# Kernel tuning notes

Hardware: AMD Instinct MI355X
Metric: run time of the kernel (lower is better)

The kernel has to match this reference:

```python
import jax, jax.numpy as jnp
import numpy as np

ARAP_WEIGHT = 1.0


def _decoder(code, W1, b1, W2, b2, W3, b3):
    # code: [D] -> vertices [N, 3]
    h = jax.nn.relu(code @ W1 + b1)
    h = jax.nn.relu(h @ W2 + b2)
    v = h @ W3 + b3
    return v.reshape(-1, 3)


def _arap_per_vertex(xyz1, recon, nbr, num_nbr, wmat):
    # xyz1, recon: [N,3]; nbr: [N,K] int; num_nbr: [N]; wmat: [N,K]
    N, K = nbr.shape
    mask = (jnp.arange(K)[None, :] < num_nbr[:, None]).astype(wmat.dtype)
    w = wmat * mask                              # zero out padded neighbors
    e_rest = xyz1[nbr] - xyz1[:, None, :]        # [N,K,3] rest-pose edges (gather)
    e_def = recon[nbr] - recon[:, None, :]       # [N,K,3] deformed edges (gather)
    # weighted covariance per vertex: S_i = sum_k w_ik e_ik e'_ik^T  -> [N,3,3]
    S = jnp.einsum('nk,nka,nkb->nab', w, e_rest, e_def)
    U, _, Vt = jnp.linalg.svd(S)
    V = jnp.swapaxes(Vt, -1, -2)
    R0 = jnp.einsum('nab,ncb->nac', V, U)        # V U^T
    d = jnp.linalg.det(R0)                       # reflection fix
    diag = jnp.stack([jnp.ones_like(d), jnp.ones_like(d), d], axis=-1)  # [N,3]
    R = jnp.einsum('nab,nb,ncb->nac', V, diag, U)
    R = jax.lax.stop_gradient(R)                 # local-global: rotations fixed in bwd
    e_rot = jnp.einsum('nab,nkb->nka', R, e_rest)
    resid = e_def - e_rot
    return jnp.sum(w * jnp.sum(resid * resid, axis=-1), axis=-1)  # [N]


def setup_inputs() -> dict:
    key = jax.random.key(0)
    ks = jax.random.split(key, 12)
    N, K, D = 20000, 16, 256
    H1, H2 = 512, 1024
    inp = {
        'code': jax.random.normal(ks[0], (D,), jnp.float32),
        'xyz1': jax.random.normal(ks[1], (N, 3), jnp.float32),
        'weightMatrix': jax.random.uniform(ks[2], (N, K), jnp.float32),
        'W1': jax.random.normal(ks[3], (D, H1), jnp.float32) * (1.0 / np.sqrt(D)),
        'b1': jax.random.normal(ks[4], (H1,), jnp.float32) * 0.01,
        'W2': jax.random.normal(ks[5], (H1, H2), jnp.float32) * (1.0 / np.sqrt(H1)),
        'b2': jax.random.normal(ks[6], (H2,), jnp.float32) * 0.01,
        'W3': jax.random.normal(ks[7], (H2, N * 3), jnp.float32) * (1.0 / np.sqrt(H2)),
        'b3': jax.random.normal(ks[8], (N * 3,), jnp.float32) * 0.01,
        'neighborsMatrix': jax.random.randint(ks[9], (N, K), 0, N, jnp.int64),
        'numNeighbors': jax.random.randint(ks[10], (N,), 0, 17, jnp.int64),
    }
    return inp


def reference(code, xyz1, weightMatrix, W1, b1, W2, b2, W3, b3,
              neighborsMatrix, numNeighbors):
    def energy(c):
        recon = _decoder(c, W1, b1, W2, b2, W3, b3)
        pv = _arap_per_vertex(xyz1, recon, neighborsMatrix, numNeighbors, weightMatrix)
        return ARAP_WEIGHT * jnp.mean(pv)

    E, g = jax.value_and_grad(energy)(code)
    # torch module returns (arapEnergy.item(), -code.grad) with arapEnergy = -E
    return (-E, g)
```

## Files before the change

### kernel.cpp

```cpp
#include <hip/hip_runtime.h>
#include <hip/hip_bf16.h>

#define N_V   20000
#define KNB   16
#define DCODE 256
#define H1    512
#define H2    1024
#define M3    60000

#define OFF_L1P   0
#define OFF_L2P   4096
#define OFF_VPART 12288
#define OFF_V     492288
#define OFF_GV    552288
#define OFF_GZ2   612288
#define OFF_GZ1   613312
#define OFF_H1    613824
#define OFF_H2    614336
#define OFF_HC    615360
#define OFF_LIST  616384
#define OFF_CNT   617408
#define OFF_E     617410
#define OFF_R     617412


__global__ void k_l1p(const float* __restrict__ code, const float* __restrict__ W1,
                      float* __restrict__ ws) {
    int m = blockIdx.x * 256 + threadIdx.x;
    int d0 = blockIdx.y * 32;
    float acc = 0.f;
#pragma unroll
    for (int d = 0; d < 32; ++d)
        acc += code[d0 + d] * W1[(size_t)(d0 + d) * H1 + m];
    ws[OFF_L1P + blockIdx.y * H1 + m] = acc;
    int gid = (blockIdx.y * 2 + blockIdx.x) * 256 + threadIdx.x;
    for (int idx = gid; idx < M3; idx += 4096) ws[OFF_GV + idx] = 0.f;
    if (gid == 0) { ws[OFF_E] = 0.f; ws[OFF_E + 1] = 0.f; }
}

__global__ void k_l2p(const float* __restrict__ b1, const float* __restrict__ W2,
                      float* __restrict__ ws) {
    __shared__ float h1s[64];
    int dz = blockIdx.y, d0 = dz * 64;
    int t = threadIdx.x;
    if (t < 64) {
        float s = b1[d0 + t];
#pragma unroll
        for (int p = 0; p < 8; ++p) s += ws[OFF_L1P + p * H1 + d0 + t];
        float h = fmaxf(s, 0.f);
        h1s[t] = h;
        if (blockIdx.x == 0) ws[OFF_H1 + d0 + t] = h;
    }
    __syncthreads();
    int m = blockIdx.x * 256 + t;
    float acc = 0.f;
#pragma unroll 8
    for (int d = 0; d < 64; ++d)
        acc += h1s[d] * W2[(size_t)(d0 + d) * H2 + m];
    ws[OFF_L2P + dz * H2 + m] = acc;
}

__global__ void k_compact(const float* __restrict__ b2, float* __restrict__ ws) {
    __shared__ int scan[256];
    int t = threadIdx.x;
    float h[4]; int c = 0;
#pragma unroll
    for (int q = 0; q < 4; ++q) {
        int j = t * 4 + q;
        float s = b2[j];
#pragma unroll
        for (int p = 0; p < 8; ++p) s += ws[OFF_L2P + p * H2 + j];
        float hv = fmaxf(s, 0.f);
        ws[OFF_H2 + j] = hv;
        ws[OFF_GZ2 + j] = 0.f;
        h[q] = hv;
        c += (hv > 0.f) ? 1 : 0;
    }
    scan[t] = c;
    __syncthreads();
    for (int off = 1; off < 256; off <<= 1) {
        int x = (t >= off) ? scan[t - off] : 0;
        __syncthreads();
        scan[t] += x;
        __syncthreads();
    }
    int base = scan[t] - c;
    int* list = reinterpret_cast<int*>(&ws[OFF_LIST]);
#pragma unroll
    for (int q = 0; q < 4; ++q) {
        if (h[q] > 0.f) {
            list[base] = t * 4 + q;
            ws[OFF_HC + base] = h[q];
            ++base;
        }
    }
    if (t == 255) *reinterpret_cast<int*>(&ws[OFF_CNT]) = scan[255];
}

__global__ void k_l3p(const float* __restrict__ W3, float* __restrict__ ws) {
    __shared__ int   rlist[128];
    __shared__ float rh[128];
    int jz = blockIdx.y;
    int cnt = *reinterpret_cast<const int*>(&ws[OFF_CNT]);
    int per = (cnt + 7) >> 3;
    int s0 = jz * per;
    int s1 = s0 + per; if (s1 > cnt) s1 = cnt;
    int n = s1 - s0;
    int t = threadIdx.x;
    if (t < 128 && t < n) {
        rlist[t] = reinterpret_cast<const int*>(&ws[OFF_LIST])[s0 + t];
        rh[t]    = ws[OFF_HC + s0 + t];
    }
    __syncthreads();
    int m4 = blockIdx.x * 1024 + t * 4;
    if (m4 >= M3) return;
    float ax = 0.f, ay = 0.f, az = 0.f, aw = 0.f;
    int ii = 0;
    for (; ii + 3 < n; ii += 4) {
        int r0 = rlist[ii], r1 = rlist[ii + 1], r2 = rlist[ii + 2], r3 = rlist[ii + 3];
        float h0 = rh[ii], h1v = rh[ii + 1], h2v = rh[ii + 2], h3 = rh[ii + 3];
        float4 w0 = *reinterpret_cast<const float4*>(&W3[(size_t)r0 * M3 + m4]);
        float4 w1 = *reinterpret_cast<const float4*>(&W3[(size_t)r1 * M3 + m4]);
        float4 w2 = *reinterpret_cast<const float4*>(&W3[(size_t)r2 * M3 + m4]);
        float4 w3 = *reinterpret_cast<const float4*>(&W3[(size_t)r3 * M3 + m4]);
        ax += h0 * w0.x + h1v * w1.x + h2v * w2.x + h3 * w3.x;
        ay += h0 * w0.y + h1v * w1.y + h2v * w2.y + h3 * w3.y;
        az += h0 * w0.z + h1v * w1.z + h2v * w2.z + h3 * w3.z;
        aw += h0 * w0.w + h1v * w1.w + h2v * w2.w + h3 * w3.w;
    }
    for (; ii < n; ++ii) {
        int r0 = rlist[ii]; float h0 = rh[ii];
        float4 w0 = *reinterpret_cast<const float4*>(&W3[(size_t)r0 * M3 + m4]);
        ax += h0 * w0.x; ay += h0 * w0.y; az += h0 * w0.z; aw += h0 * w0.w;
    }
    float4 acc = make_float4(ax, ay, az, aw);
    *reinterpret_cast<float4*>(&ws[OFF_VPART + jz * M3 + m4]) = acc;
}

__global__ void k_vred(const float* __restrict__ b3, float* __restrict__ ws) {
    int i4 = blockIdx.x * 256 + threadIdx.x;
    if (i4 < M3 / 4) {
        int m = i4 * 4;
        float4 a = *reinterpret_cast<const float4*>(&b3[m]);
#pragma unroll
        for (int jz = 0; jz < 8; ++jz) {
            float4 p = *reinterpret_cast<const float4*>(&ws[OFF_VPART + jz * M3 + m]);
            a.x += p.x; a.y += p.y; a.z += p.z; a.w += p.w;
        }
        *reinterpret_cast<float4*>(&ws[OFF_V + m]) = a;
    }
}


__device__ inline void jrotf(float a[3][3], float v[3][3], int p, int q) {
    float apq = a[p][q];
    if (fabsf(apq) < 1e-30f) return;
    float theta = (a[q][q] - a[p][p]) / (2.0f * apq);
    float t;
    if (fabsf(theta) > 1e18f) t = 0.5f / theta;
    else t = copysignf(1.0f, theta) / (fabsf(theta) + sqrtf(theta * theta + 1.0f));
    float c = 1.0f / sqrtf(t * t + 1.0f);
    float s = t * c;
    float app = a[p][p], aqq = a[q][q];
    a[p][p] = app - t * apq;
    a[q][q] = aqq + t * apq;
    a[p][q] = 0.0f; a[q][p] = 0.0f;
    int r = 3 - p - q;
    float arp = a[r][p], arq = a[r][q];
    a[r][p] = c * arp - s * arq; a[p][r] = a[r][p];
    a[r][q] = s * arp + c * arq; a[q][r] = a[r][q];
#pragma unroll
    for (int k2 = 0; k2 < 3; ++k2) {
        float vkp = v[k2][p], vkq = v[k2][q];
        v[k2][p] = c * vkp - s * vkq;
        v[k2][q] = s * vkp + c * vkq;
    }
}

__device__ void compute_Rf(const float S[3][3], float R[3][3]) {
    float A[3][3], V[3][3];
#pragma unroll
    for (int a = 0; a < 3; ++a)
#pragma unroll
        for (int b = 0; b < 3; ++b) {
            float s = 0.0f;
#pragma unroll
            for (int c = 0; c < 3; ++c) s += S[c][a] * S[c][b];
            A[a][b] = s;
            V[a][b] = (a == b) ? 1.0f : 0.0f;
        }
    for (int sweep = 0; sweep < 15; ++sweep) {
        float off = A[0][1]*A[0][1] + A[0][2]*A[0][2] + A[1][2]*A[1][2];
        float dg  = A[0][0]*A[0][0] + A[1][1]*A[1][1] + A[2][2]*A[2][2];
        if (off <= 1e-12f * (dg + 1e-30f)) break;
        jrotf(A, V, 0, 1); jrotf(A, V, 0, 2); jrotf(A, V, 1, 2);
    }
    int id[3] = {0, 1, 2};
    if (A[id[0]][id[0]] < A[id[1]][id[1]]) { int t = id[0]; id[0] = id[1]; id[1] = t; }
    if (A[id[0]][id[0]] < A[id[2]][id[2]]) { int t = id[0]; id[0] = id[2]; id[2] = t; }
    if (A[id[1]][id[1]] < A[id[2]][id[2]]) { int t = id[1]; id[1] = id[2]; id[2] = t; }
    float v0[3], v1[3], v2[3];
#pragma unroll
    for (int r = 0; r < 3; ++r) {
        v0[r] = V[r][id[0]]; v1[r] = V[r][id[1]]; v2[r] = V[r][id[2]];
    }
    float u0[3], u1[3], u2[3];
#pragma unroll
    for (int a = 0; a < 3; ++a)
        u0[a] = S[a][0]*v0[0] + S[a][1]*v0[1] + S[a][2]*v0[2];
    float n0 = sqrtf(u0[0]*u0[0] + u0[1]*u0[1] + u0[2]*u0[2]);
    if (!(n0 > 1e-20f)) {
#pragma unroll
        for (int a = 0; a < 3; ++a)
#pragma unroll
            for (int c = 0; c < 3; ++c) R[a][c] = (a == c) ? 1.0f : 0.0f;
        return;
    }
#pragma unroll
    for (int a = 0; a < 3; ++a) u0[a] /= n0;
    float t1[3];
#pragma unroll
    for (int a = 0; a < 3; ++a)
        t1[a] = S[a][0]*v1[0] + S[a][1]*v1[1] + S[a][2]*v1[2];
    float dp = u0[0]*t1[0] + u0[1]*t1[1] + u0[2]*t1[2];
#pragma unroll
    for (int a = 0; a < 3; ++a) t1[a] -= dp * u0[a];
    float n1 = sqrtf(t1[0]*t1[0] + t1[1]*t1[1] + t1[2]*t1[2]);
    if (n1 > 1e-5f * n0) {
#pragma unroll
        for (int a = 0; a < 3; ++a) u1[a] = t1[a] / n1;
    } else {
        int m = (fabsf(u0[0]) <= fabsf(u0[1]) && fabsf(u0[0]) <= fabsf(u0[2])) ? 0
              : (fabsf(u0[1]) <= fabsf(u0[2]) ? 1 : 2);
        float e[3] = {0.0f, 0.0f, 0.0f}; e[m] = 1.0f;
        float cx[3] = { u0[1]*e[2] - u0[2]*e[1],
                        u0[2]*e[0] - u0[0]*e[2],
                        u0[0]*e[1] - u0[1]*e[0] };
        float nn = sqrtf(cx[0]*cx[0] + cx[1]*cx[1] + cx[2]*cx[2]);
#pragma unroll
        for (int a = 0; a < 3; ++a) u1[a] = cx[a] / nn;
    }
    u2[0] = u0[1]*u1[2] - u0[2]*u1[1];
    u2[1] = u0[2]*u1[0] - u0[0]*u1[2];
    u2[2] = u0[0]*u1[1] - u0[1]*u1[0];
    float d = v0[0]*(v1[1]*v2[2] - v1[2]*v2[1])
            - v0[1]*(v1[0]*v2[2] - v1[2]*v2[0])
            + v0[2]*(v1[0]*v2[1] - v1[1]*v2[0]);
#pragma unroll
    for (int a = 0; a < 3; ++a)
#pragma unroll
        for (int c = 0; c < 3; ++c)
            R[a][c] = v0[a]*u0[c] + v1[a]*u1[c] + d * (v2[a]*u2[c]);
}

__global__ void k_arapR(const float* __restrict__ xyz1, const float* __restrict__ wmat,
                        const int* __restrict__ nbr, const int* __restrict__ nnum,
                        float* __restrict__ ws) {
    int i = blockIdx.x * 64 + threadIdx.x;
    if (i >= N_V) return;
    const float* recon = ws + OFF_V;
    int num = nnum[i]; if (num > KNB) num = KNB;
    float cr0 = xyz1[3*i], cr1 = xyz1[3*i+1], cr2 = xyz1[3*i+2];
    float cd0 = recon[3*i], cd1 = recon[3*i+1], cd2 = recon[3*i+2];
    float S[3][3] = {{0,0,0},{0,0,0},{0,0,0}};
    for (int k = 0; k < num; ++k) {
        int j = nbr[i*KNB + k];
        float w = wmat[i*KNB + k];
        float er0 = xyz1[3*j]   - cr0, er1 = xyz1[3*j+1] - cr1, er2 = xyz1[3*j+2] - cr2;
        float ed0 = recon[3*j]  - cd0, ed1 = recon[3*j+1] - cd1, ed2 = recon[3*j+2] - cd2;
        S[0][0] += w*er0*ed0; S[0][1] += w*er0*ed1; S[0][2] += w*er0*ed2;
        S[1][0] += w*er1*ed0; S[1][1] += w*er1*ed1; S[1][2] += w*er1*ed2;
        S[2][0] += w*er2*ed0; S[2][1] += w*er2*ed1; S[2][2] += w*er2*ed2;
    }
    float R[3][3];
    compute_Rf(S, R);
#pragma unroll
    for (int a = 0; a < 3; ++a)
#pragma unroll
        for (int c = 0; c < 3; ++c)
            ws[OFF_R + (a*3 + c) * N_V + i] = R[a][c];
}

__global__ void k_arapG(const float* __restrict__ xyz1, const float* __restrict__ wmat,
                        const int* __restrict__ nbr, const int* __restrict__ nnum,
                        float* __restrict__ ws) {
    const float* recon = ws + OFF_V;
    float* gv = ws + OFF_GV;
    int i = blockIdx.x * 64 + threadIdx.x;
    double pv = 0.0;
    if (i < N_V) {
        int num = nnum[i]; if (num > KNB) num = KNB;
        float cr0 = xyz1[3*i], cr1 = xyz1[3*i+1], cr2 = xyz1[3*i+2];
        float cd0 = recon[3*i], cd1 = recon[3*i+1], cd2 = recon[3*i+2];
        float R00 = ws[OFF_R + 0*N_V + i], R01 = ws[OFF_R + 1*N_V + i], R02 = ws[OFF_R + 2*N_V + i];
        float R10 = ws[OFF_R + 3*N_V + i], R11 = ws[OFF_R + 4*N_V + i], R12 = ws[OFF_R + 5*N_V + i];
        float R20 = ws[OFF_R + 6*N_V + i], R21 = ws[OFF_R + 7*N_V + i], R22 = ws[OFF_R + 8*N_V + i];
        const float gscale = 2.0f / (float)N_V;
        float own0 = 0.f, own1 = 0.f, own2 = 0.f;
        for (int k = 0; k < num; ++k) {
            int j = nbr[i*KNB + k];
            float w = wmat[i*KNB + k];
            float er0 = xyz1[3*j]   - cr0, er1 = xyz1[3*j+1] - cr1, er2 = xyz1[3*j+2] - cr2;
            float ed0 = recon[3*j]  - cd0, ed1 = recon[3*j+1] - cd1, ed2 = recon[3*j+2] - cd2;
            float r0 = ed0 - (R00*er0 + R01*er1 + R02*er2);
            float r1 = ed1 - (R10*er0 + R11*er1 + R12*er2);
            float r2 = ed2 - (R20*er0 + R21*er1 + R22*er2);
            pv += (double)(w * (r0*r0 + r1*r1 + r2*r2));
            float g0 = gscale * w * r0;
            float g1 = gscale * w * r1;
            float g2 = gscale * w * r2;
            atomicAdd(&gv[3*j+0], g0);
            atomicAdd(&gv[3*j+1], g1);
            atomicAdd(&gv[3*j+2], g2);
            own0 += g0; own1 += g1; own2 += g2;
        }
        if (num > 0) {
            atomicAdd(&gv[3*i+0], -own0);
            atomicAdd(&gv[3*i+1], -own1);
            atomicAdd(&gv[3*i+2], -own2);
        }
    }
#pragma unroll
    for (int m = 32; m; m >>= 1) pv += __shfl_xor(pv, m);
    if (threadIdx.x == 0)
        atomicAdd(reinterpret_cast<double*>(ws + OFF_E), pv);
}


__global__ void k_gh2(const float* __restrict__ W3, float* __restrict__ ws) {
    int b = blockIdx.x;
    int cnt = *reinterpret_cast<const int*>(&ws[OFF_CNT]);
    if (b >= cnt) return;
    int j = reinterpret_cast<const int*>(&ws[OFF_LIST])[b];
    const float4* w3r = reinterpret_cast<const float4*>(W3 + (size_t)j * M3);
    const float4* gv4 = reinterpret_cast<const float4*>(ws + OFF_GV);
    float acc = 0.f;
    for (int it = threadIdx.x; it < M3 / 4; it += 256) {
        float4 a = w3r[it], g = gv4[it];
        acc += a.x*g.x + a.y*g.y + a.z*g.z + a.w*g.w;
    }
    for (int m = 32; m; m >>= 1) acc += __shfl_xor(acc, m);
    __shared__ float wsum[4];
    if ((threadIdx.x & 63) == 0) wsum[threadIdx.x >> 6] = acc;
    __syncthreads();
    if (threadIdx.x == 0) ws[OFF_GZ2 + j] = wsum[0] + wsum[1] + wsum[2] + wsum[3];
}

__global__ void k_gh1(const float* __restrict__ W2, float* __restrict__ ws) {
    int wv = threadIdx.x >> 6, ln = threadIdx.x & 63;
    int i = blockIdx.x * 4 + wv;
    const float* gz2 = ws + OFF_GZ2;
    float acc = 0.f;
#pragma unroll
    for (int it = 0; it < H2 / 64; ++it) {
        int jj = ln + it * 64;
        acc += W2[(size_t)i * H2 + jj] * gz2[jj];
    }
    for (int m = 32; m; m >>= 1) acc += __shfl_xor(acc, m);
    if (ln == 0) ws[OFF_GZ1 + i] = (ws[OFF_H1 + i] > 0.f) ? acc : 0.f;
}

__global__ void k_gcode(const float* __restrict__ W1, float* __restrict__ ws,
                        float* __restrict__ out) {
    int wv = threadIdx.x >> 6, ln = threadIdx.x & 63;
    int d = blockIdx.x * 4 + wv;
    const float* gz1 = ws + OFF_GZ1;
    float acc = 0.f;
#pragma unroll
    for (int it = 0; it < H1 / 64; ++it) {
        int ii = ln + it * 64;
        acc += W1[(size_t)d * H1 + ii] * gz1[ii];
    }
    for (int m = 32; m; m >>= 1) acc += __shfl_xor(acc, m);
    if (ln == 0) out[1 + d] = acc;
    if (blockIdx.x == 0 && threadIdx.x == 0) {
        double E = *reinterpret_cast<const double*>(ws + OFF_E);
        out[0] = (float)(-(E / (double)N_V));
    }
}

extern "C" void kernel_launch(void* const* d_in, const int* in_sizes, int n_in,
                              void* d_out, int out_size, void* d_ws, size_t ws_size,
                              hipStream_t stream) {
    const float* code = (const float*)d_in[0];
    const float* xyz1 = (const float*)d_in[1];
    const float* wmat = (const float*)d_in[2];
    const float* W1   = (const float*)d_in[3];
    const float* b1   = (const float*)d_in[4];
    const float* W2   = (const float*)d_in[5];
    const float* b2   = (const float*)d_in[6];
    const float* W3   = (const float*)d_in[7];
    const float* b3   = (const float*)d_in[8];
    const int*   nbr  = (const int*)d_in[9];
    const int*   nnum = (const int*)d_in[10];
    float* out = (float*)d_out;
    float* ws  = (float*)d_ws;

    k_l1p    <<<dim3(2, 8),  256, 0, stream>>>(code, W1, ws);
    k_l2p    <<<dim3(4, 8),  256, 0, stream>>>(b1, W2, ws);
    k_compact<<<1,           256, 0, stream>>>(b2, ws);
    k_l3p    <<<dim3(59, 8), 256, 0, stream>>>(W3, ws);
    k_vred   <<<59,          256, 0, stream>>>(b3, ws);
    k_arapR  <<<313,          64, 0, stream>>>(xyz1, wmat, nbr, nnum, ws);
    k_arapG  <<<313,          64, 0, stream>>>(xyz1, wmat, nbr, nnum, ws);
    k_gh2    <<<1024,        256, 0, stream>>>(W3, ws);
    k_gh1    <<<128,         256, 0, stream>>>(W2, ws);
    k_gcode  <<<64,          256, 0, stream>>>(W1, ws, out);
}
```

Before: 120.9 us.

## Fuse decoder and ARAP stages to cut kernel launches from ten to six

Result: slower. 143.2 us (+18.4%).

```diff
diff --git a/kernel.cpp b/kernel.cpp
--- a/kernel.cpp
+++ b/kernel.cpp
@@ -8,110 +8,86 @@
 #define H2    1024
 #define M3    60000
 
-#define OFF_L1P   0
-#define OFF_L2P   4096
-#define OFF_VPART 12288
-#define OFF_V     492288
-#define OFF_GV    552288
-#define OFF_GZ2   612288
-#define OFF_GZ1   613312
-#define OFF_H1    613824
-#define OFF_H2    614336
-#define OFF_HC    615360
-#define OFF_LIST  616384
-#define OFF_CNT   617408
-#define OFF_E     617410
-#define OFF_R     617412
-
-
-__global__ void k_l1p(const float* __restrict__ code, const float* __restrict__ W1,
+#define OFF_V     0
+#define OFF_GV    60000
+#define OFF_GZ2   120000
+#define OFF_GZ1   121024
+#define OFF_H1    121536
+#define OFF_H2    122048
+#define OFF_E     123072
+
+__global__ void k_mlp(const float* __restrict__ code, const float* __restrict__ W1,
+                      const float* __restrict__ b1, const float* __restrict__ W2,
+                      const float* __restrict__ b2, const float* __restrict__ b3,
                       float* __restrict__ ws) {
-    int m = blockIdx.x * 256 + threadIdx.x;
-    int d0 = blockIdx.y * 32;
+    __shared__ float h1s[H1];
+    __shared__ float zp[8][32];
+    int t = threadIdx.x;
+
+    for (int mm = t; mm < H1; mm += 256) {
+        float acc = 0.f;
+#pragma unroll 4
+        for (int d = 0; d < DCODE; ++d)
+            acc += code[d] * W1[(size_t)d * H1 + mm];
+        h1s[mm] = fmaxf(acc + b1[mm], 0.f);
+    }
+    __syncthreads();
+    if (blockIdx.x == 0)
+        for (int mm = t; mm < H1; mm += 256) ws[OFF_H1 + mm] = h1s[mm];
+
+    int g = t >> 5, mm = t & 31;
+    int m = blockIdx.x * 32 + mm;
     float acc = 0.f;
-#pragma unroll
-    for (int d = 0; d < 32; ++d)
-        acc += code[d0 + d] * W1[(size_t)(d0 + d) * H1 + m];
-    ws[OFF_L1P + blockIdx.y * H1 + m] = acc;
-    int gid = (blockIdx.y * 2 + blockIdx.x) * 256 + threadIdx.x;
-    for (int idx = gid; idx < M3; idx += 4096) ws[OFF_GV + idx] = 0.f;
+    int d0 = g * 64;
+#pragma unroll 8
+    for (int d = d0; d < d0 + 64; ++d)
+        acc += h1s[d] * W2[(size_t)d * H2 + m];
+    zp[g][mm] = acc;
+    __syncthreads();
+    if (g == 0) {
+        float s = b2[m];
+#pragma unroll
+        for (int p = 0; p < 8; ++p) s += zp[p][mm];
+        ws[OFF_H2 + m] = fmaxf(s, 0.f);
+    }
+
+    int gid = blockIdx.x * 256 + t;
+    for (int idx = gid; idx < M3; idx += 8192) {
+        ws[OFF_V + idx]  = b3[idx];
+        ws[OFF_GV + idx] = 0.f;
+    }
     if (gid == 0) { ws[OFF_E] = 0.f; ws[OFF_E + 1] = 0.f; }
 }
 
-__global__ void k_l2p(const float* __restrict__ b1, const float* __restrict__ W2,
-                      float* __restrict__ ws) {
-    __shared__ float h1s[64];
-    int dz = blockIdx.y, d0 = dz * 64;
+__global__ void k_l3v(const float* __restrict__ W3, float* __restrict__ ws) {
+    __shared__ float rh[128];
+    __shared__ int   rlist[128];
+    __shared__ int   scan[128];
     int t = threadIdx.x;
-    if (t < 64) {
-        float s = b1[d0 + t];
-#pragma unroll
-        for (int p = 0; p < 8; ++p) s += ws[OFF_L1P + p * H1 + d0 + t];
-        float h = fmaxf(s, 0.f);
-        h1s[t] = h;
-        if (blockIdx.x == 0) ws[OFF_H1 + d0 + t] = h;
-    }
-    __syncthreads();
-    int m = blockIdx.x * 256 + t;
-    float acc = 0.f;
-#pragma unroll 8
-    for (int d = 0; d < 64; ++d)
-        acc += h1s[d] * W2[(size_t)(d0 + d) * H2 + m];
-    ws[OFF_L2P + dz * H2 + m] = acc;
-}
-
-__global__ void k_compact(const float* __restrict__ b2, float* __restrict__ ws) {
-    __shared__ int scan[256];
-    int t = threadIdx.x;
-    float h[4]; int c = 0;
-#pragma unroll
-    for (int q = 0; q < 4; ++q) {
-        int j = t * 4 + q;
-        float s = b2[j];
-#pragma unroll
-        for (int p = 0; p < 8; ++p) s += ws[OFF_L2P + p * H2 + j];
-        float hv = fmaxf(s, 0.f);
-        ws[OFF_H2 + j] = hv;
-        ws[OFF_GZ2 + j] = 0.f;
-        h[q] = hv;
-        c += (hv > 0.f) ? 1 : 0;
-    }
-    scan[t] = c;
-    __syncthreads();
-    for (int off = 1; off < 256; off <<= 1) {
-        int x = (t >= off) ? scan[t - off] : 0;
+    int rbase = blockIdx.y * 128;
+
+    float hv = 0.f; int flag = 0;
+    if (t < 128) {
+        hv = ws[OFF_H2 + rbase + t];
+        flag = (hv > 0.f) ? 1 : 0;
+        scan[t] = flag;
+    }
+    __syncthreads();
+    for (int off = 1; off < 128; off <<= 1) {
+        int x = 0;
+        if (t < 128 && t >= off) x = scan[t - off];
         __syncthreads();
-        scan[t] += x;
+        if (t < 128) scan[t] += x;
         __syncthreads();
     }
-    int base = scan[t] - c;
-    int* list = reinterpret_cast<int*>(&ws[OFF_LIST]);
-#pragma unroll
-    for (int q = 0; q < 4; ++q) {
-        if (h[q] > 0.f) {
-            list[base] = t * 4 + q;
-            ws[OFF_HC + base] = h[q];
-            ++base;
-        }
-    }
-    if (t == 255) *reinterpret_cast<int*>(&ws[OFF_CNT]) = scan[255];
-}
-
-__global__ void k_l3p(const float* __restrict__ W3, float* __restrict__ ws) {
-    __shared__ int   rlist[128];
-    __shared__ float rh[128];
-    int jz = blockIdx.y;
-    int cnt = *reinterpret_cast<const int*>(&ws[OFF_CNT]);
-    int per = (cnt + 7) >> 3;
-    int s0 = jz * per;
-    int s1 = s0 + per; if (s1 > cnt) s1 = cnt;
-    int n = s1 - s0;
-    int t = threadIdx.x;
-    if (t < 128 && t < n) {
-        rlist[t] = reinterpret_cast<const int*>(&ws[OFF_LIST])[s0 + t];
-        rh[t]    = ws[OFF_HC + s0 + t];
-    }
-    __syncthreads();
+    if (t < 128 && flag) {
+        int idx = scan[t] - 1;
+        rlist[idx] = rbase + t;
+        rh[idx] = hv;
+    }
+    __syncthreads();
+    int n = scan[127];
+
     int m4 = blockIdx.x * 1024 + t * 4;
     if (m4 >= M3) return;
     float ax = 0.f, ay = 0.f, az = 0.f, aw = 0.f;
@@ -133,22 +109,10 @@
         float4 w0 = *reinterpret_cast<const float4*>(&W3[(size_t)r0 * M3 + m4]);
         ax += h0 * w0.x; ay += h0 * w0.y; az += h0 * w0.z; aw += h0 * w0.w;
     }
-    float4 acc = make_float4(ax, ay, az, aw);
-    *reinterpret_cast<float4*>(&ws[OFF_VPART + jz * M3 + m4]) = acc;
-}
-
-__global__ void k_vred(const float* __restrict__ b3, float* __restrict__ ws) {
-    int i4 = blockIdx.x * 256 + threadIdx.x;
-    if (i4 < M3 / 4) {
-        int m = i4 * 4;
-        float4 a = *reinterpret_cast<const float4*>(&b3[m]);
-#pragma unroll
-        for (int jz = 0; jz < 8; ++jz) {
-            float4 p = *reinterpret_cast<const float4*>(&ws[OFF_VPART + jz * M3 + m]);
-            a.x += p.x; a.y += p.y; a.z += p.z; a.w += p.w;
-        }
-        *reinterpret_cast<float4*>(&ws[OFF_V + m]) = a;
-    }
+    atomicAdd(&ws[OFF_V + m4 + 0], ax);
+    atomicAdd(&ws[OFF_V + m4 + 1], ay);
+    atomicAdd(&ws[OFF_V + m4 + 2], az);
+    atomicAdd(&ws[OFF_V + m4 + 3], aw);
 }
 
 
@@ -253,37 +217,9 @@
             R[a][c] = v0[a]*u0[c] + v1[a]*u1[c] + d * (v2[a]*u2[c]);
 }
 
-__global__ void k_arapR(const float* __restrict__ xyz1, const float* __restrict__ wmat,
-                        const int* __restrict__ nbr, const int* __restrict__ nnum,
-                        float* __restrict__ ws) {
-    int i = blockIdx.x * 64 + threadIdx.x;
-    if (i >= N_V) return;
-    const float* recon = ws + OFF_V;
-    int num = nnum[i]; if (num > KNB) num = KNB;
-    float cr0 = xyz1[3*i], cr1 = xyz1[3*i+1], cr2 = xyz1[3*i+2];
-    float cd0 = recon[3*i], cd1 = recon[3*i+1], cd2 = recon[3*i+2];
-    float S[3][3] = {{0,0,0},{0,0,0},{0,0,0}};
-    for (int k = 0; k < num; ++k) {
-        int j = nbr[i*KNB + k];
-        float w = wmat[i*KNB + k];
-        float er0 = xyz1[3*j]   - cr0, er1 = xyz1[3*j+1] - cr1, er2 = xyz1[3*j+2] - cr2;
-        float ed0 = recon[3*j]  - cd0, ed1 = recon[3*j+1] - cd1, ed2 = recon[3*j+2] - cd2;
-        S[0][0] += w*er0*ed0; S[0][1] += w*er0*ed1; S[0][2] += w*er0*ed2;
-        S[1][0] += w*er1*ed0; S[1][1] += w*er1*ed1; S[1][2] += w*er1*ed2;
-        S[2][0] += w*er2*ed0; S[2][1] += w*er2*ed1; S[2][2] += w*er2*ed2;
-    }
-    float R[3][3];
-    compute_Rf(S, R);
-#pragma unroll
-    for (int a = 0; a < 3; ++a)
-#pragma unroll
-        for (int c = 0; c < 3; ++c)
-            ws[OFF_R + (a*3 + c) * N_V + i] = R[a][c];
-}
-
-__global__ void k_arapG(const float* __restrict__ xyz1, const float* __restrict__ wmat,
-                        const int* __restrict__ nbr, const int* __restrict__ nnum,
-                        float* __restrict__ ws) {
+__global__ void k_arap(const float* __restrict__ xyz1, const float* __restrict__ wmat,
+                       const int* __restrict__ nbr, const int* __restrict__ nnum,
+                       float* __restrict__ ws) {
     const float* recon = ws + OFF_V;
     float* gv = ws + OFF_GV;
     int i = blockIdx.x * 64 + threadIdx.x;
@@ -292,19 +228,28 @@
         int num = nnum[i]; if (num > KNB) num = KNB;
         float cr0 = xyz1[3*i], cr1 = xyz1[3*i+1], cr2 = xyz1[3*i+2];
         float cd0 = recon[3*i], cd1 = recon[3*i+1], cd2 = recon[3*i+2];
-        float R00 = ws[OFF_R + 0*N_V + i], R01 = ws[OFF_R + 1*N_V + i], R02 = ws[OFF_R + 2*N_V + i];
-        float R10 = ws[OFF_R + 3*N_V + i], R11 = ws[OFF_R + 4*N_V + i], R12 = ws[OFF_R + 5*N_V + i];
-        float R20 = ws[OFF_R + 6*N_V + i], R21 = ws[OFF_R + 7*N_V + i], R22 = ws[OFF_R + 8*N_V + i];
+        float S[3][3] = {{0,0,0},{0,0,0},{0,0,0}};
+        for (int k = 0; k < num; ++k) {
+            int j = nbr[i*KNB + k];
+            float w = wmat[i*KNB + k];
+            float er0 = xyz1[3*j]  - cr0, er1 = xyz1[3*j+1] - cr1, er2 = xyz1[3*j+2] - cr2;
+            float ed0 = recon[3*j] - cd0, ed1 = recon[3*j+1] - cd1, ed2 = recon[3*j+2] - cd2;
+            S[0][0] += w*er0*ed0; S[0][1] += w*er0*ed1; S[0][2] += w*er0*ed2;
+            S[1][0] += w*er1*ed0; S[1][1] += w*er1*ed1; S[1][2] += w*er1*ed2;
+            S[2][0] += w*er2*ed0; S[2][1] += w*er2*ed1; S[2][2] += w*er2*ed2;
+        }
+        float R[3][3];
+        compute_Rf(S, R);
         const float gscale = 2.0f / (float)N_V;
         float own0 = 0.f, own1 = 0.f, own2 = 0.f;
         for (int k = 0; k < num; ++k) {
             int j = nbr[i*KNB + k];
             float w = wmat[i*KNB + k];
-            float er0 = xyz1[3*j]   - cr0, er1 = xyz1[3*j+1] - cr1, er2 = xyz1[3*j+2] - cr2;
-            float ed0 = recon[3*j]  - cd0, ed1 = recon[3*j+1] - cd1, ed2 = recon[3*j+2] - cd2;
-            float r0 = ed0 - (R00*er0 + R01*er1 + R02*er2);
-            float r1 = ed1 - (R10*er0 + R11*er1 + R12*er2);
-            float r2 = ed2 - (R20*er0 + R21*er1 + R22*er2);
+            float er0 = xyz1[3*j]  - cr0, er1 = xyz1[3*j+1] - cr1, er2 = xyz1[3*j+2] - cr2;
+            float ed0 = recon[3*j] - cd0, ed1 = recon[3*j+1] - cd1, ed2 = recon[3*j+2] - cd2;
+            float r0 = ed0 - (R[0][0]*er0 + R[0][1]*er1 + R[0][2]*er2);
+            float r1 = ed1 - (R[1][0]*er0 + R[1][1]*er1 + R[1][2]*er2);
+            float r2 = ed2 - (R[2][0]*er0 + R[2][1]*er1 + R[2][2]*er2);
             pv += (double)(w * (r0*r0 + r1*r1 + r2*r2));
             float g0 = gscale * w * r0;
             float g1 = gscale * w * r1;
@@ -328,10 +273,12 @@
 
 
 __global__ void k_gh2(const float* __restrict__ W3, float* __restrict__ ws) {
-    int b = blockIdx.x;
-    int cnt = *reinterpret_cast<const int*>(&ws[OFF_CNT]);
-    if (b >= cnt) return;
-    int j = reinterpret_cast<const int*>(&ws[OFF_LIST])[b];
+    int j = blockIdx.x;
+    float h2v = ws[OFF_H2 + j];
+    if (h2v <= 0.f) {
+        if (threadIdx.x == 0) ws[OFF_GZ2 + j] = 0.f;
+        return;
+    }
     const float4* w3r = reinterpret_cast<const float4*>(W3 + (size_t)j * M3);
     const float4* gv4 = reinterpret_cast<const float4*>(ws + OFF_GV);
     float acc = 0.f;
@@ -396,14 +343,10 @@
     float* out = (float*)d_out;
     float* ws  = (float*)d_ws;
 
-    k_l1p    <<<dim3(2, 8),  256, 0, stream>>>(code, W1, ws);
-    k_l2p    <<<dim3(4, 8),  256, 0, stream>>>(b1, W2, ws);
-    k_compact<<<1,           256, 0, stream>>>(b2, ws);
-    k_l3p    <<<dim3(59, 8), 256, 0, stream>>>(W3, ws);
-    k_vred   <<<59,          256, 0, stream>>>(b3, ws);
-    k_arapR  <<<313,          64, 0, stream>>>(xyz1, wmat, nbr, nnum, ws);
-    k_arapG  <<<313,          64, 0, stream>>>(xyz1, wmat, nbr, nnum, ws);
-    k_gh2    <<<1024,        256, 0, stream>>>(W3, ws);
-    k_gh1    <<<128,         256, 0, stream>>>(W2, ws);
-    k_gcode  <<<64,          256, 0, stream>>>(W1, ws, out);
-}
+    k_mlp  <<<32,          256, 0, stream>>>(code, W1, b1, W2, b2, b3, ws);
+    k_l3v  <<<dim3(59, 8), 256, 0, stream>>>(W3, ws);
+    k_arap <<<313,          64, 0, stream>>>(xyz1, wmat, nbr, nnum, ws);
+    k_gh2  <<<1024,        256, 0, stream>>>(W3, ws);
+    k_gh1  <<<128,         256, 0, stream>>>(W2, ws);
+    k_gcode<<<64,          256, 0, stream>>>(W1, ws, out);
+}
```
